# Kernel tuning notes

Hardware: AMD Instinct MI355X
Metric: run time of the kernel (lower is better)

The kernel has to match this reference:

```python
import jax, jax.numpy as jnp
import numpy as np

VOCAB = 32000
DIM = 1024
BATCH = 2
SEQ = 2048
CHUNK = 256
LCTX = 4            # local_context_size, mode='sum'
LOCAL_WIN = 512     # sparse_local_window (>= 2*chunk)
GSTRIDE = 1024      # sparse_global_stride (>= 4*chunk)
LN_EPS = 1e-5


def _cache_positions():
    """Simulate the deterministic sparse KV-cache pruning per chunk (numpy, trace-time).
    Returns list of key-position index arrays (cached positions ++ current chunk)."""
    cache = np.zeros((0,), dtype=np.int64)
    per_chunk = []
    for i in range(SEQ // CHUNK):
        new = np.arange(i * CHUNK, (i + 1) * CHUNK, dtype=np.int64)
        full = np.concatenate([cache, new])
        per_chunk.append(full)
        total_seen = (i + 1) * CHUNK
        local_start = max(0, total_seen - LOCAL_WIN)
        keep = (full >= local_start) | (full % GSTRIDE == 0)
        cache = full[keep]
    return per_chunk


def setup_inputs() -> dict:
    key = jax.random.key(0)
    ks = jax.random.split(key, 8)
    s = 0.02
    return {
        "x": jax.random.randint(ks[0], (BATCH, SEQ), 0, VOCAB, dtype=jnp.int64),
        "emb_table": jax.random.normal(ks[1], (VOCAB, DIM), jnp.float32) * s,
        "q_w": jax.random.normal(ks[2], (DIM, DIM), jnp.float32) * s,
        "q_b": jnp.zeros((DIM,), jnp.float32),
        "k_w": jax.random.normal(ks[3], (DIM, DIM), jnp.float32) * s,
        "k_b": jnp.zeros((DIM,), jnp.float32),
        "v_w": jax.random.normal(ks[4], (DIM, DIM), jnp.float32) * s,
        "v_b": jnp.zeros((DIM,), jnp.float32),
        "o_w": jax.random.normal(ks[5], (DIM, DIM), jnp.float32) * s,
        "o_b": jnp.zeros((DIM,), jnp.float32),
        "ln_w": jnp.ones((DIM,), jnp.float32),
        "ln_b": jnp.zeros((DIM,), jnp.float32),
        "out_w": jax.random.normal(ks[6], (VOCAB, DIM), jnp.float32) * s,
        "out_b": jnp.zeros((VOCAB,), jnp.float32),
    }


def reference(x, emb_table, q_w, q_b, k_w, k_b, v_w, v_b, o_w, o_b, ln_w, ln_b, out_w, out_b):
    # embedding + causal local context (sum of 0..LCTX-1 shifted embeddings)
    emb = emb_table[x]                                  # [B,S,D]
    ctx = emb
    for off in range(1, LCTX):
        ctx = ctx + jnp.pad(emb, ((0, 0), (off, 0), (0, 0)))[:, :SEQ]

    # project full sequence once (same per-chunk projections in the original)
    Q = ctx @ q_w.T + q_b                               # [B,S,D]
    K = ctx @ k_w.T + k_b
    V = ctx @ v_w.T + v_b
    scale = 1.0 / np.sqrt(DIM).astype(np.float32)

    outs = []
    for i, kpos in enumerate(_cache_positions()):
        qpos = np.arange(i * CHUNK, (i + 1) * CHUNK, dtype=np.int64)
        q = Q[:, i * CHUNK:(i + 1) * CHUNK]             # [B,C,D]
        k = K[:, kpos]                                  # [B,Ki,D] gathered sparse cache + chunk
        v = V[:, kpos]
        scores = jnp.einsum('bqd,bkd->bqk', q, k) * scale
        mask = kpos[None, :] > qpos[:, None]            # [C,Ki] static causal mask
        scores = jnp.where(mask[None, :, :], -jnp.inf, scores)
        w = jax.nn.softmax(scores, axis=-1)
        outs.append(jnp.einsum('bqk,bkd->bqd', w, v))

    attended = jnp.concatenate(outs, axis=1)            # [B,S,D]
    h = attended @ o_w.T + o_b
    # LayerNorm
    mu = h.mean(-1, keepdims=True)
    var = ((h - mu) ** 2).mean(-1, keepdims=True)
    h = (h - mu) / jnp.sqrt(var + LN_EPS) * ln_w + ln_b
    return h @ out_w.T + out_b                          # [B,S,VOCAB]
```

## Files before the change

kernel.cpp:

```cpp
#include <hip/hip_runtime.h>
#include <stdint.h>

#define DIMN 1024
#define SEQN 2048
#define BATCHN 2
#define NCHUNK 8
#define CHUNKSZ 256
#define VOCABN 32000
#define ROWS_PB 6016
#define PSTRIDE_B (256*ROWS_PB)
#define LN_EPS 1e-5f

#define MBIG 4096
#define NBIG 32000
#define KBIG 1024
#define NTILES_K (KBIG/64)

typedef unsigned short ushort_t;
typedef __attribute__((ext_vector_type(8))) __bf16 bf16x8;
typedef __attribute__((ext_vector_type(4))) float f32x4;

__device__ const int d_nk[8]   = {256,512,768,769,769,769,769,770};
__device__ const int d_np[8]   = {256,512,768,896,896,896,896,896};
__device__ const int d_koff[8] = {0,256,768,1536,2432,3328,4224,5120};

__device__ __forceinline__ ushort_t f2bu(float f) {
  union { float f; unsigned u; } v; v.f = f;
  unsigned r = v.u + 0x7FFFu + ((v.u >> 16) & 1u);
  return (ushort_t)(r >> 16);
}
__device__ __forceinline__ float b2f(ushort_t u) {
  union { unsigned u; float f; } v; v.u = ((unsigned)u) << 16; return v.f;
}

__device__ __forceinline__ int pos_of(int i, int j) {
  if (i <= 2) return j;
  if (i <= 6) return (j == 0) ? 0 : (i - 3) * 256 + 255 + j;
  return (j == 0) ? 0 : ((j == 1) ? 1024 : 1278 + j);
}

__device__ __forceinline__ void gload16(const void* g, void* l) {
  __builtin_amdgcn_global_load_lds((__attribute__((address_space(1))) void*)g,
                                   (__attribute__((address_space(3))) void*)l,
                                   16, 0, 0);
}

__device__ __forceinline__ void mma_core_s(const ushort_t* __restrict__ A,
                                           const ushort_t* __restrict__ Bt,
                                           int K, ushort_t* lA, ushort_t* lB,
                                           f32x4 acc[4][4], int tid) {
  const int lane = tid & 63;
  const int wr = (tid >> 7) & 1;
  const int wc = (tid >> 6) & 1;
  const int frow = lane & 15;
  const int lhi = lane >> 4;
  const int xk = (frow & 7) << 4;
  const size_t ldb = (size_t)K * 2;
  for (int kt = 0; kt < K; kt += 64) {
#pragma unroll
    for (int t = 0; t < 4; ++t) {
      int cid = t * 256 + tid;
      int row = cid >> 3;
      int srcoff = ((cid & 7) * 16) ^ ((row & 7) << 4);
      gload16((const char*)A  + (size_t)row * ldb + (size_t)kt * 2 + srcoff,
              (char*)lA + cid * 16);
      gload16((const char*)Bt + (size_t)row * ldb + (size_t)kt * 2 + srcoff,
              (char*)lB + cid * 16);
    }
    __syncthreads();
#pragma unroll
    for (int kk = 0; kk < 2; ++kk) {
      bf16x8 af[4], bfr[4];
#pragma unroll
      for (int m = 0; m < 4; ++m) {
        int r = wr * 64 + m * 16 + frow;
        af[m] = *(const bf16x8*)((const char*)lA +
                 ((r * 128 + kk * 64 + lhi * 16) ^ xk));
      }
#pragma unroll
      for (int n = 0; n < 4; ++n) {
        int r = wc * 64 + n * 16 + frow;
        bfr[n] = *(const bf16x8*)((const char*)lB +
                  ((r * 128 + kk * 64 + lhi * 16) ^ xk));
      }
#pragma unroll
      for (int m = 0; m < 4; ++m)
#pragma unroll
        for (int n = 0; n < 4; ++n)
          acc[m][n] = __builtin_amdgcn_mfma_f32_16x16x32_bf16(af[m], bfr[n],
                                                              acc[m][n], 0, 0, 0);
    }
    __syncthreads();
  }
}

__device__ __forceinline__ void stage_tile_big(const char* Abase, const char* Bbase,
                                               ushort_t* ldsbuf, int ktile, int tid) {
  const size_t ldb = (size_t)KBIG * 2;
#pragma unroll
  for (int s = 0; s < 4; ++s) {
    const char* base = (s < 2 ? Abase : Bbase) + (size_t)(s & 1) * 128 * ldb
                       + (size_t)ktile * 128;
    ushort_t* lh = ldsbuf + s * 8192;
#pragma unroll
    for (int r2 = 0; r2 < 2; ++r2) {
      int c = r2 * 512 + tid;
      int row = c >> 3;
      int off_l = (c * 16) ^ ((row & 7) << 4);
      gload16(base + (size_t)row * ldb + (off_l & 127), (char*)lh + c * 16);
    }
  }
}

__global__ __launch_bounds__(512, 2) void k_vocab(
    const ushort_t* __restrict__ A, const ushort_t* __restrict__ Bt,
    const float* __restrict__ bias, float* __restrict__ C) {
  __shared__ ushort_t lds[2][4][8192];
  const int tid = threadIdx.x;
  const int lane = tid & 63, w = tid >> 6, wm = w >> 2, wn = w & 3;
  const int frow = lane & 15, lhi = lane >> 4;
  const int xk = (frow & 7) << 4;

  int l = blockIdx.x;
  int loc = l >> 3;
  int mh  = loc / 125;
  const int mt = (l & 7) * 2 + mh;
  const int nt = loc - mh * 125;
  const char* Abase = (const char*)(A + (size_t)mt * 256 * KBIG);
  const char* Bbase = (const char*)(Bt + (size_t)nt * 256 * KBIG);

  f32x4 acc[8][4] = {};

  stage_tile_big(Abase, Bbase, &lds[0][0][0], 0, tid);

  for (int kt = 0; kt < NTILES_K; ++kt) {
    const int cur = kt & 1;
    __builtin_amdgcn_sched_barrier(0);
    if (kt + 1 < NTILES_K) {
      stage_tile_big(Abase, Bbase, &lds[cur ^ 1][0][0], kt + 1, tid);
      asm volatile("s_waitcnt vmcnt(8)");
    } else {
      asm volatile("s_waitcnt vmcnt(0)");
    }
    __builtin_amdgcn_s_barrier();
    __builtin_amdgcn_sched_barrier(0);

    const char* lA = (const char*)&lds[cur][wm][0];
    const char* lB = (const char*)&lds[cur][2 + (wn >> 1)][0];

    bf16x8 bF[4][2];
#pragma unroll
    for (int fc = 0; fc < 4; ++fc) {
      int c = (wn & 1) * 64 + fc * 16 + frow;
#pragma unroll
      for (int kk = 0; kk < 2; ++kk)
        bF[fc][kk] = *(const bf16x8*)(lB + ((c * 128 + kk * 64 + lhi * 16) ^ xk));
    }
#pragma unroll
    for (int q = 0; q < 4; ++q) {
      bf16x8 aF[2][2];
#pragma unroll
      for (int i = 0; i < 2; ++i) {
        int r = (2 * q + i) * 16 + frow;
#pragma unroll
        for (int kk = 0; kk < 2; ++kk)
          aF[i][kk] = *(const bf16x8*)(lA + ((r * 128 + kk * 64 + lhi * 16) ^ xk));
      }
      if (q) __builtin_amdgcn_s_barrier();
      __builtin_amdgcn_s_setprio(1);
#pragma unroll
      for (int i = 0; i < 2; ++i)
#pragma unroll
        for (int fc = 0; fc < 4; ++fc)
#pragma unroll
          for (int kk = 0; kk < 2; ++kk)
            acc[2 * q + i][fc] = __builtin_amdgcn_mfma_f32_16x16x32_bf16(
                aF[i][kk], bF[fc][kk], acc[2 * q + i][fc], 0, 0, 0);
      __builtin_amdgcn_s_setprio(0);
    }
    __builtin_amdgcn_s_barrier();
  }

  const int rbase = mt * 256 + wm * 128 + lhi * 4;
  const int cbase = nt * 256 + wn * 64 + frow;
#pragma unroll
  for (int fc = 0; fc < 4; ++fc) {
    float bv = bias[cbase + fc * 16];
#pragma unroll
    for (int fr = 0; fr < 8; ++fr)
#pragma unroll
      for (int j = 0; j < 4; ++j)
        __builtin_nontemporal_store(acc[fr][fc][j] + bv,
            &C[(size_t)(rbase + fr * 16 + j) * NBIG + cbase + fc * 16]);
  }
}

#define SEG (DIMN*DIMN/4)
__global__ __launch_bounds__(256) void k_cvt5(
    const float* __restrict__ qw, const float* __restrict__ kw,
    const float* __restrict__ vw, const float* __restrict__ ow,
    const float* __restrict__ outw, ushort_t* __restrict__ wqkvb,
    ushort_t* __restrict__ wob, ushort_t* __restrict__ woutb) {
  const int total = 4 * SEG + (VOCABN * DIMN / 4);
  int idx = blockIdx.x * 256 + threadIdx.x;
  int stride = gridDim.x * 256;
  for (int i = idx; i < total; i += stride) {
    const float4* src; ushort4* dst;
    if (i < 3 * SEG) {
      src = (const float4*)(i < SEG ? qw : i < 2 * SEG ? kw : vw) +
            (i - (i < SEG ? 0 : i < 2 * SEG ? SEG : 2 * SEG));
      dst = (ushort4*)wqkvb + i;
    } else if (i < 4 * SEG) {
      src = (const float4*)ow + (i - 3 * SEG);
      dst = (ushort4*)wob + (i - 3 * SEG);
    } else {
      src = (const float4*)outw + (i - 4 * SEG);
      dst = (ushort4*)woutb + (i - 4 * SEG);
    }
    float4 v = *src;
    *dst = make_ushort4(f2bu(v.x), f2bu(v.y), f2bu(v.z), f2bu(v.w));
  }
}

__global__ __launch_bounds__(256) void k_embed(const int* __restrict__ x,
                                               const float* __restrict__ emb,
                                               ushort_t* __restrict__ ctxb) {
  const int t = blockIdx.x, b = blockIdx.y, tid = threadIdx.x;
  float4 s = make_float4(0.f, 0.f, 0.f, 0.f);
#pragma unroll
  for (int o = 0; o < 4; ++o) {
    if (t - o < 0) break;
    int tok = x[b * SEQN + t - o];
    float4 v = ((const float4*)(emb + (size_t)tok * DIMN))[tid];
    s.x += v.x; s.y += v.y; s.z += v.z; s.w += v.w;
  }
  ((ushort4*)(ctxb + ((size_t)(b * SEQN + t)) * DIMN))[tid] =
      make_ushort4(f2bu(s.x), f2bu(s.y), f2bu(s.z), f2bu(s.w));
}

__global__ __launch_bounds__(256) void k_qkv(const ushort_t* __restrict__ A,
    const ushort_t* __restrict__ Bt, const float* __restrict__ qb2,
    const float* __restrict__ kb2, const float* __restrict__ vb2,
    ushort_t* __restrict__ Qb, ushort_t* __restrict__ Kb,
    ushort_t* __restrict__ Vb) {
  int l = blockIdx.x;
  int swz = (l & 7) * ((int)gridDim.x >> 3) + (l >> 3);
  const int mt = swz & 31;
  const int nt = swz >> 5;
  __shared__ __align__(16) ushort_t lA[128*64];
  __shared__ __align__(16) ushort_t lB[128*64];
  f32x4 acc[4][4] = {};
  const int tid = threadIdx.x;
  mma_core_s(A + (size_t)mt * 128 * KBIG,
             Bt + (size_t)nt * 128 * KBIG, KBIG, lA, lB, acc, tid);
  const int which = nt >> 3;
  const int col0  = (nt & 7) * 128;
  ushort_t* Out = (which == 0) ? Qb : (which == 1) ? Kb : Vb;
  const float* Bv = (which == 0) ? qb2 : (which == 1) ? kb2 : vb2;
  const int lane = tid & 63, wr = (tid >> 7) & 1, wc = (tid >> 6) & 1;
  const int rbase = mt * 128 + wr * 64 + (lane >> 4) * 4;
  const int cbase = col0 + wc * 64 + (lane & 15);
#pragma unroll
  for (int m = 0; m < 4; ++m)
#pragma unroll
    for (int n = 0; n < 4; ++n) {
      int c = cbase + n * 16;
      float bv = Bv[c];
#pragma unroll
      for (int j = 0; j < 4; ++j)
        Out[(size_t)(rbase + m * 16 + j) * DIMN + c] = f2bu(acc[m][n][j] + bv);
    }
}

__global__ __launch_bounds__(256) void k_oproj(const ushort_t* __restrict__ A,
    const ushort_t* __restrict__ Bt, const float* __restrict__ bias,
    ushort_t* __restrict__ C) {
  __shared__ __align__(16) ushort_t lA[128*64];
  __shared__ __align__(16) ushort_t lB[128*64];
  f32x4 acc[4][4] = {};
  const int tid = threadIdx.x;
  mma_core_s(A + (size_t)blockIdx.y * 128 * KBIG,
             Bt + (size_t)blockIdx.x * 128 * KBIG, KBIG, lA, lB, acc, tid);
  const int lane = tid & 63, wr = (tid >> 7) & 1, wc = (tid >> 6) & 1;
  const int rbase = blockIdx.y * 128 + wr * 64 + (lane >> 4) * 4;
  const int cbase = blockIdx.x * 128 + wc * 64 + (lane & 15);
#pragma unroll
  for (int m = 0; m < 4; ++m)
#pragma unroll
    for (int n = 0; n < 4; ++n) {
      int c = cbase + n * 16;
      float bv = bias[c];
#pragma unroll
      for (int j = 0; j < 4; ++j)
        C[(size_t)(rbase + m * 16 + j) * DIMN + c] = f2bu(acc[m][n][j] + bv);
    }
}

__global__ __launch_bounds__(256) void k_transV(const ushort_t* __restrict__ Vb,
                                                ushort_t* __restrict__ VgT) {
  __shared__ ushort_t tile[64][66];
  const int z = blockIdx.z, b = z >> 3, i = z & 7;
  const int np = d_np[i], nk = d_nk[i], ko = d_koff[i];
  const int jb = blockIdx.x * 64;
  if (jb >= np) return;
  const int db = blockIdx.y * 64;
  const int tid = threadIdx.x, tx = tid & 63, ty = tid >> 6;
#pragma unroll
  for (int rep = 0; rep < 16; ++rep) {
    int jl = rep * 4 + ty;
    int j = jb + jl;
    ushort_t v = 0;
    if (j < nk) v = Vb[((size_t)b * SEQN + pos_of(i, j)) * DIMN + db + tx];
    tile[jl][tx] = v;
  }
  __syncthreads();
  const size_t base = ((size_t)b * ROWS_PB + ko) * DIMN;
#pragma unroll
  for (int rep = 0; rep < 16; ++rep) {
    int dl = rep * 4 + ty;
    VgT[base + (size_t)(db + dl) * np + jb + tx] = tile[tx][dl];
  }
}

__global__ __launch_bounds__(256) void k_scores(const ushort_t* __restrict__ Qb,
    const ushort_t* __restrict__ Kb, ushort_t* __restrict__ P) {
  const int z = blockIdx.z, b = z >> 3, i = z & 7;
  const int np = d_np[i], nk = d_nk[i], ko = d_koff[i];
  if ((int)blockIdx.x * 128 >= np) return;
  __shared__ __align__(16) ushort_t lA[128*64];
  __shared__ __align__(16) ushort_t lB[128*64];
  f32x4 acc[4][4] = {};
  const int tid = threadIdx.x;
  const int lane = tid & 63, wr = (tid >> 7) & 1, wc = (tid >> 6) & 1;
  const int frow = lane & 15, lhi = lane >> 4;
  const int xk = (frow & 7) << 4;

  const char* sA[4]; const char* sB[4];
  {
    const char* Aq = (const char*)(Qb +
        ((size_t)(b * SEQN + i * CHUNKSZ) + blockIdx.y * 128) * DIMN);
#pragma unroll
    for (int t = 0; t < 4; ++t) {
      int cid = t * 256 + tid;
      int row = cid >> 3;
      int srcoff = ((cid & 7) * 16) ^ ((row & 7) << 4);
      sA[t] = Aq + (size_t)row * 2048 + srcoff;
      int jg = blockIdx.x * 128 + row;
      int pos = (jg < nk) ? pos_of(i, jg) : 0;
      sB[t] = (const char*)(Kb + ((size_t)b * SEQN + pos) * DIMN) + srcoff;
    }
  }

  for (int kt = 0; kt < KBIG; kt += 64) {
#pragma unroll
    for (int t = 0; t < 4; ++t) {
      int cid = t * 256 + tid;
      gload16(sA[t] + (size_t)kt * 2, (char*)lA + cid * 16);
      gload16(sB[t] + (size_t)kt * 2, (char*)lB + cid * 16);
    }
    __syncthreads();
#pragma unroll
    for (int kk = 0; kk < 2; ++kk) {
      bf16x8 af[4], bfr[4];
#pragma unroll
      for (int m = 0; m < 4; ++m) {
        int r = wr * 64 + m * 16 + frow;
        af[m] = *(const bf16x8*)((const char*)lA +
                 ((r * 128 + kk * 64 + lhi * 16) ^ xk));
      }
#pragma unroll
      for (int n = 0; n < 4; ++n) {
        int r = wc * 64 + n * 16 + frow;
        bfr[n] = *(const bf16x8*)((const char*)lB +
                  ((r * 128 + kk * 64 + lhi * 16) ^ xk));
      }
#pragma unroll
      for (int m = 0; m < 4; ++m)
#pragma unroll
        for (int n = 0; n < 4; ++n)
          acc[m][n] = __builtin_amdgcn_mfma_f32_16x16x32_bf16(af[m], bfr[n],
                                                              acc[m][n], 0, 0, 0);
    }
    __syncthreads();
  }

  const int rb = blockIdx.y * 128 + wr * 64 + (lane >> 4) * 4;
  const int cb = blockIdx.x * 128 + wc * 64 + (lane & 15);
  ushort_t* Pc = P + (size_t)b * PSTRIDE_B + (size_t)ko * 256;
  const float scale = 0.03125f;
  const int diag0 = nk - CHUNKSZ;
#pragma unroll
  for (int m = 0; m < 4; ++m)
#pragma unroll
    for (int n = 0; n < 4; ++n) {
      int c = cb + n * 16;
#pragma unroll
      for (int j = 0; j < 4; ++j) {
        int r = rb + m * 16 + j;
        float w = 0.0f;
        if (c < nk && (c - diag0) <= r) w = expf(acc[m][n][j] * scale);
        Pc[(size_t)r * np + c] = f2bu(w);
      }
    }
}

__global__ __launch_bounds__(256) void k_rowsum(const ushort_t* __restrict__ P,
                                                float* __restrict__ rowsum) {
  const int z = blockIdx.y, b = z >> 3, i = z & 7, r = blockIdx.x;
  const int np = d_np[i], ko = d_koff[i];
  const ushort_t* row = P + (size_t)b * PSTRIDE_B + (size_t)ko * 256 + (size_t)r * np;
  const int tid = threadIdx.x;
  float s = 0.f;
  for (int c = tid; c < np; c += 256) s += b2f(row[c]);
#pragma unroll
  for (int o = 1; o < 64; o <<= 1) s += __shfl_xor(s, o);
  __shared__ float ss[4];
  if ((tid & 63) == 0) ss[tid >> 6] = s;
  __syncthreads();
  if (tid == 0) rowsum[z * 256 + r] = ss[0] + ss[1] + ss[2] + ss[3];
}

__global__ __launch_bounds__(256) void k_pv(const ushort_t* __restrict__ P,
    const ushort_t* __restrict__ VgT, const float* __restrict__ rowsum,
    ushort_t* __restrict__ attb) {
  const int z = blockIdx.z, b = z >> 3, i = z & 7;
  const int np = d_np[i], ko = d_koff[i];
  __shared__ __align__(16) ushort_t lA[128*64];
  __shared__ __align__(16) ushort_t lB[128*64];
  f32x4 acc[4][4] = {};
  const int tid = threadIdx.x;
  const ushort_t* A  = P + (size_t)b * PSTRIDE_B + (size_t)ko * 256 +
                       (size_t)blockIdx.y * 128 * np;
  const ushort_t* Bt = VgT + ((size_t)b * ROWS_PB + ko) * DIMN +
                       (size_t)blockIdx.x * 128 * np;
  mma_core_s(A, Bt, np, lA, lB, acc, tid);
  const int lane = tid & 63, wr = (tid >> 7) & 1, wc = (tid >> 6) & 1;
  const int rb = blockIdx.y * 128 + wr * 64 + (lane >> 4) * 4;
  const int cb = blockIdx.x * 128 + wc * 64 + (lane & 15);
  const float* rs = rowsum + z * 256;
  ushort_t* outp = attb + (size_t)(b * SEQN + i * CHUNKSZ) * DIMN;
#pragma unroll
  for (int m = 0; m < 4; ++m)
#pragma unroll
    for (int j = 0; j < 4; ++j) {
      int r = rb + m * 16 + j;
      float inv = 1.0f / rs[r];
#pragma unroll
      for (int n = 0; n < 4; ++n)
        outp[(size_t)r * DIMN + cb + n * 16] = f2bu(acc[m][n][j] * inv);
    }
}

__global__ __launch_bounds__(256) void k_ln(const ushort_t* __restrict__ h,
    const float* __restrict__ lnw, const float* __restrict__ lnb,
    ushort_t* __restrict__ hb) {
  const int row = blockIdx.x, tid = threadIdx.x;
  ushort4 u4 = ((const ushort4*)(h + (size_t)row * DIMN))[tid];
  float4 v = make_float4(b2f(u4.x), b2f(u4.y), b2f(u4.z), b2f(u4.w));
  float s  = v.x + v.y + v.z + v.w;
  float sq = v.x * v.x + v.y * v.y + v.z * v.z + v.w * v.w;
#pragma unroll
  for (int o = 1; o < 64; o <<= 1) { s += __shfl_xor(s, o); sq += __shfl_xor(sq, o); }
  __shared__ float ss[4], ssq[4];
  if ((tid & 63) == 0) { ss[tid >> 6] = s; ssq[tid >> 6] = sq; }
  __syncthreads();
  s  = ss[0] + ss[1] + ss[2] + ss[3];
  sq = ssq[0] + ssq[1] + ssq[2] + ssq[3];
  const float mu  = s * (1.0f / DIMN);
  const float var = sq * (1.0f / DIMN) - mu * mu;
  const float inv = rsqrtf(var + LN_EPS);
  float4 w4 = ((const float4*)lnw)[tid];
  float4 b4 = ((const float4*)lnb)[tid];
  ushort4 o4 = make_ushort4(f2bu((v.x - mu) * inv * w4.x + b4.x),
                            f2bu((v.y - mu) * inv * w4.y + b4.y),
                            f2bu((v.z - mu) * inv * w4.z + b4.z),
                            f2bu((v.w - mu) * inv * w4.w + b4.w));
  ((ushort4*)(hb + (size_t)row * DIMN))[tid] = o4;
}

extern "C" void kernel_launch(void* const* d_in, const int* in_sizes, int n_in,
                              void* d_out, int out_size, void* d_ws, size_t ws_size,
                              hipStream_t stream) {
  const int*   x    = (const int*)  d_in[0];
  const float* emb  = (const float*)d_in[1];
  const float* qw   = (const float*)d_in[2];
  const float* qb   = (const float*)d_in[3];
  const float* kw   = (const float*)d_in[4];
  const float* kb   = (const float*)d_in[5];
  const float* vw   = (const float*)d_in[6];
  const float* vb   = (const float*)d_in[7];
  const float* ow   = (const float*)d_in[8];
  const float* ob   = (const float*)d_in[9];
  const float* lnw  = (const float*)d_in[10];
  const float* lnb  = (const float*)d_in[11];
  const float* outw = (const float*)d_in[12];
  const float* outb = (const float*)d_in[13];
  float* out = (float*)d_out;
  (void)in_sizes; (void)n_in; (void)out_size; (void)ws_size;

  char* ws = (char*)d_ws;
  size_t off = 0;
  auto alloc = [&](size_t bytes) {
    size_t r = off; off += (bytes + 255) & ~(size_t)255; return r;
  };
  ushort_t* wqkvb = (ushort_t*)(ws + alloc((size_t)3 * DIMN * DIMN * 2));
  ushort_t* wob   = (ushort_t*)(ws + alloc((size_t)DIMN * DIMN * 2));
  ushort_t* woutb = (ushort_t*)(ws + alloc((size_t)VOCABN * DIMN * 2));
  ushort_t* ctxb  = (ushort_t*)(ws + alloc((size_t)BATCHN * SEQN * DIMN * 2));
  ushort_t* Qb    = (ushort_t*)(ws + alloc((size_t)BATCHN * SEQN * DIMN * 2));
  ushort_t* Kb    = (ushort_t*)(ws + alloc((size_t)BATCHN * SEQN * DIMN * 2));
  ushort_t* Vb    = (ushort_t*)(ws + alloc((size_t)BATCHN * SEQN * DIMN * 2));
  ushort_t* VgT   = (ushort_t*)(ws + alloc((size_t)BATCHN * ROWS_PB * DIMN * 2));
  ushort_t* Pm    = (ushort_t*)(ws + alloc((size_t)BATCHN * PSTRIDE_B * 2));
  float*    rsum  = (float*)   (ws + alloc((size_t)BATCHN * NCHUNK * 256 * 4));
  ushort_t* attb  = (ushort_t*)(ws + alloc((size_t)BATCHN * SEQN * DIMN * 2));
  ushort_t* hbuf  = (ushort_t*)(ws + alloc((size_t)BATCHN * SEQN * DIMN * 2));
  ushort_t* hb    = (ushort_t*)(ws + alloc((size_t)BATCHN * SEQN * DIMN * 2));

  k_cvt5<<<dim3(4096), dim3(256), 0, stream>>>(qw, kw, vw, ow, outw,
                                               wqkvb, wob, woutb);

  k_embed<<<dim3(SEQN, BATCHN), dim3(256), 0, stream>>>(x, emb, ctxb);

  k_qkv<<<dim3(768), dim3(256), 0, stream>>>(ctxb, wqkvb, qb, kb, vb,
                                             Qb, Kb, Vb);

  k_transV<<<dim3(14, 16, BATCHN * NCHUNK), dim3(256), 0, stream>>>(Vb, VgT);

  k_scores<<<dim3(7, 2, BATCHN * NCHUNK), dim3(256), 0, stream>>>(Qb, Kb, Pm);
  k_rowsum<<<dim3(256, BATCHN * NCHUNK), dim3(256), 0, stream>>>(Pm, rsum);
  k_pv<<<dim3(8, 2, BATCHN * NCHUNK), dim3(256), 0, stream>>>(Pm, VgT, rsum, attb);

  k_oproj<<<dim3(8, 32), dim3(256), 0, stream>>>(attb, wob, ob, hbuf);
  k_ln<<<dim3(BATCHN * SEQN), dim3(256), 0, stream>>>(hbuf, lnw, lnb, hb);

  k_vocab<<<dim3(2000), dim3(512), 0, stream>>>(hb, woutb, outb, out);
}
```

Baseline: 512.5 us.

## Retile vocab GEMM to 256x128 tiles with k=32 steps and higher occupancy

```diff
diff --git a/kernel.cpp b/kernel.cpp
--- a/kernel.cpp
+++ b/kernel.cpp
@@ -14,7 +14,6 @@
 #define MBIG 4096
 #define NBIG 32000
 #define KBIG 1024
-#define NTILES_K (KBIG/64)
 
 typedef unsigned short ushort_t;
 typedef __attribute__((ext_vector_type(8))) __bf16 bf16x8;
@@ -94,104 +93,103 @@
   }
 }
 
-__device__ __forceinline__ void stage_tile_big(const char* Abase, const char* Bbase,
-                                               ushort_t* ldsbuf, int ktile, int tid) {
-  const size_t ldb = (size_t)KBIG * 2;
-#pragma unroll
-  for (int s = 0; s < 4; ++s) {
-    const char* base = (s < 2 ? Abase : Bbase) + (size_t)(s & 1) * 128 * ldb
-                       + (size_t)ktile * 128;
-    ushort_t* lh = ldsbuf + s * 8192;
-#pragma unroll
-    for (int r2 = 0; r2 < 2; ++r2) {
-      int c = r2 * 512 + tid;
-      int row = c >> 3;
-      int off_l = (c * 16) ^ ((row & 7) << 4);
-      gload16(base + (size_t)row * ldb + (off_l & 127), (char*)lh + c * 16);
-    }
-  }
-}
-
-__global__ __launch_bounds__(512, 2) void k_vocab(
+__global__ __launch_bounds__(512, 4) void k_vocab2(
     const ushort_t* __restrict__ A, const ushort_t* __restrict__ Bt,
     const float* __restrict__ bias, float* __restrict__ C) {
-  __shared__ ushort_t lds[2][4][8192];
+  __shared__ ushort_t lds[2][12288];
   const int tid = threadIdx.x;
-  const int lane = tid & 63, w = tid >> 6, wm = w >> 2, wn = w & 3;
+  const int lane = tid & 63, w = tid >> 6;
+  const int wm = w >> 1, wn = w & 1;
   const int frow = lane & 15, lhi = lane >> 4;
-  const int xk = (frow & 7) << 4;
 
   int l = blockIdx.x;
   int loc = l >> 3;
-  int mh  = loc / 125;
+  int mh = loc / 250;
   const int mt = (l & 7) * 2 + mh;
-  const int nt = loc - mh * 125;
-  const char* Abase = (const char*)(A + (size_t)mt * 256 * KBIG);
-  const char* Bbase = (const char*)(Bt + (size_t)nt * 256 * KBIG);
-
-  f32x4 acc[8][4] = {};
-
-  stage_tile_big(Abase, Bbase, &lds[0][0][0], 0, tid);
-
-  for (int kt = 0; kt < NTILES_K; ++kt) {
-    const int cur = kt & 1;
+  const int nt = loc - mh * 250;
+
+  const char* srcs[3];
+  int dsts[3];
+  {
+    const char* Ab = (const char*)(A + (size_t)mt * 256 * KBIG);
+    const char* Bb = (const char*)(Bt + (size_t)nt * 128 * KBIG);
+#pragma unroll
+    for (int j = 0; j < 3; ++j) {
+      int c = j * 512 + tid;
+      int isB = (c >= 1024) ? 1 : 0;
+      int g = c - isB * 1024;
+      int pr = g >> 3, cp = g & 7;
+      int lc = cp ^ (pr & 7);
+      int r  = pr * 2 + (lc >> 2);
+      int kc = lc & 3;
+      srcs[j] = (isB ? Bb : Ab) + (size_t)r * 2048 + kc * 16;
+      dsts[j] = isB * 16384 + g * 16;
+    }
+  }
+
+  int aOff[4], bOff[4];
+#pragma unroll
+  for (int m = 0; m < 4; ++m) {
+    int r = wm * 64 + m * 16 + frow;
+    int pr = r >> 1, cc = (r & 1) * 4 + lhi;
+    aOff[m] = pr * 128 + ((cc * 16) ^ ((pr & 7) << 4));
+  }
+#pragma unroll
+  for (int n = 0; n < 4; ++n) {
+    int r = wn * 64 + n * 16 + frow;
+    int pr = r >> 1, cc = (r & 1) * 4 + lhi;
+    bOff[n] = 16384 + pr * 128 + ((cc * 16) ^ ((pr & 7) << 4));
+  }
+
+  f32x4 acc[4][4] = {};
+
+#define STG2(buf_, t_)                                                   \
+  { char* d_ = (char*)&lds[buf_][0];                                     \
+    _Pragma("unroll")                                                    \
+    for (int j_ = 0; j_ < 3; ++j_)                                       \
+      gload16(srcs[j_] + (size_t)(t_) * 64, d_ + dsts[j_]); }
+
+  STG2(0, 0);
+  for (int t = 0; t < 32; ++t) {
+    const int cur = t & 1;
     __builtin_amdgcn_sched_barrier(0);
-    if (kt + 1 < NTILES_K) {
-      stage_tile_big(Abase, Bbase, &lds[cur ^ 1][0][0], kt + 1, tid);
-      asm volatile("s_waitcnt vmcnt(8)");
+    if (t + 1 < 32) {
+      STG2(cur ^ 1, t + 1);
+      asm volatile("s_waitcnt vmcnt(3)");
     } else {
       asm volatile("s_waitcnt vmcnt(0)");
     }
     __builtin_amdgcn_s_barrier();
     __builtin_amdgcn_sched_barrier(0);
-
-    const char* lA = (const char*)&lds[cur][wm][0];
-    const char* lB = (const char*)&lds[cur][2 + (wn >> 1)][0];
-
-    bf16x8 bF[4][2];
-#pragma unroll
-    for (int fc = 0; fc < 4; ++fc) {
-      int c = (wn & 1) * 64 + fc * 16 + frow;
-#pragma unroll
-      for (int kk = 0; kk < 2; ++kk)
-        bF[fc][kk] = *(const bf16x8*)(lB + ((c * 128 + kk * 64 + lhi * 16) ^ xk));
-    }
-#pragma unroll
-    for (int q = 0; q < 4; ++q) {
-      bf16x8 aF[2][2];
-#pragma unroll
-      for (int i = 0; i < 2; ++i) {
-        int r = (2 * q + i) * 16 + frow;
-#pragma unroll
-        for (int kk = 0; kk < 2; ++kk)
-          aF[i][kk] = *(const bf16x8*)(lA + ((r * 128 + kk * 64 + lhi * 16) ^ xk));
-      }
-      if (q) __builtin_amdgcn_s_barrier();
-      __builtin_amdgcn_s_setprio(1);
-#pragma unroll
-      for (int i = 0; i < 2; ++i)
-#pragma unroll
-        for (int fc = 0; fc < 4; ++fc)
-#pragma unroll
-          for (int kk = 0; kk < 2; ++kk)
-            acc[2 * q + i][fc] = __builtin_amdgcn_mfma_f32_16x16x32_bf16(
-                aF[i][kk], bF[fc][kk], acc[2 * q + i][fc], 0, 0, 0);
-      __builtin_amdgcn_s_setprio(0);
-    }
+    const char* bufp = (const char*)&lds[cur][0];
+    bf16x8 aF[4], bF[4];
+#pragma unroll
+    for (int n = 0; n < 4; ++n) bF[n] = *(const bf16x8*)(bufp + bOff[n]);
+#pragma unroll
+    for (int m = 0; m < 4; ++m) aF[m] = *(const bf16x8*)(bufp + aOff[m]);
+    __builtin_amdgcn_s_setprio(1);
+#pragma unroll
+    for (int m = 0; m < 4; ++m)
+#pragma unroll
+      for (int n = 0; n < 4; ++n)
+        acc[m][n] = __builtin_amdgcn_mfma_f32_16x16x32_bf16(aF[m], bF[n],
+                                                            acc[m][n], 0, 0, 0);
+    __builtin_amdgcn_s_setprio(0);
     __builtin_amdgcn_s_barrier();
   }
-
-  const int rbase = mt * 256 + wm * 128 + lhi * 4;
-  const int cbase = nt * 256 + wn * 64 + frow;
-#pragma unroll
-  for (int fc = 0; fc < 4; ++fc) {
-    float bv = bias[cbase + fc * 16];
-#pragma unroll
-    for (int fr = 0; fr < 8; ++fr)
+#undef STG2
+
+  const int rbase = mt * 256 + wm * 64 + lhi * 4;
+  const int cbase = nt * 128 + wn * 64 + frow;
+#pragma unroll
+  for (int n = 0; n < 4; ++n) {
+    float bv = bias[cbase + n * 16];
+#pragma unroll
+    for (int m = 0; m < 4; ++m)
 #pragma unroll
       for (int j = 0; j < 4; ++j)
-        __builtin_nontemporal_store(acc[fr][fc][j] + bv,
-            &C[(size_t)(rbase + fr * 16 + j) * NBIG + cbase + fc * 16]);
+        __builtin_nontemporal_store(acc[m][n][j] + bv,
+            &C[(size_t)(rbase + m * 16 + j) * NBIG + cbase + n * 16]);
   }
 }
 
@@ -534,5 +532,5 @@
   k_oproj<<<dim3(8, 32), dim3(256), 0, stream>>>(attb, wob, ob, hbuf);
   k_ln<<<dim3(BATCHN * SEQN), dim3(256), 0, stream>>>(hbuf, lnw, lnb, hb);
 
-  k_vocab<<<dim3(2000), dim3(512), 0, stream>>>(hb, woutb, outb, out);
-}
+  k_vocab2<<<dim3(4000), dim3(512), 0, stream>>>(hb, woutb, outb, out);
+}
```

Result: no change. 510.2 us (median of 3 runs) (-0.5%).
